# Kernel optimization log

Hardware: AMD Instinct MI355X
Metric: run time of the kernel (lower is better)

## Reference

```python
import jax, jax.numpy as jnp
from jax import lax
import numpy as np

IMG = 640
C = 20  # num_classes
A = 3   # anchors per scale
LB, LO, LC = 0.05, 1.0, 0.5
ANCHORS = jnp.asarray(np.array([[(10, 13), (16, 30), (33, 23)],
                                [(30, 61), (62, 45), (59, 119)],
                                [(116, 90), (156, 198), (373, 326)]], dtype=np.float32) / IMG)


def bce_logits_mean(x, z):
    # BCEWithLogitsLoss (pos_weight=1): mean over all elements, numerically stable
    return jnp.mean(jnp.maximum(x, 0.0) - x * z + jnp.log1p(jnp.exp(-jnp.abs(x))))


def iou_cxcywh(b1, b2, eps=1e-7):
    # b1, b2: [..., 4] in (cx, cy, w, h)
    b1x1 = b1[..., 0] - b1[..., 2] / 2; b1y1 = b1[..., 1] - b1[..., 3] / 2
    b1x2 = b1[..., 0] + b1[..., 2] / 2; b1y2 = b1[..., 1] + b1[..., 3] / 2
    b2x1 = b2[..., 0] - b2[..., 2] / 2; b2y1 = b2[..., 1] - b2[..., 3] / 2
    b2x2 = b2[..., 0] + b2[..., 2] / 2; b2y2 = b2[..., 1] + b2[..., 3] / 2
    iw = jnp.clip(jnp.minimum(b1x2, b2x2) - jnp.maximum(b1x1, b2x1), 0.0)
    ih = jnp.clip(jnp.minimum(b1y2, b2y2) - jnp.maximum(b1y1, b2y1), 0.0)
    inter = iw * ih
    union = (b1x2 - b1x1) * (b1y2 - b1y1) + (b2x2 - b2x1) * (b2y2 - b2y1) - inter + eps
    return inter / union


def build_target(targets, anchors, stride, H, W):
    # targets: [N, T, 6] = (x1, y1, x2, y2, obj, cls); anchors: [A, 2]
    N, T, _ = targets.shape
    x1, y1, x2, y2 = targets[..., 0], targets[..., 1], targets[..., 2], targets[..., 3]
    cls = targets[..., 5]
    valid = (x2 > x1) & (y2 > y1)
    cx = (x1 + x2) * 0.5; cy = (y1 + y2) * 0.5
    bw = x2 - x1; bh = y2 - y1
    gx = jnp.clip(cx / stride, 0.0, W - 1).astype(jnp.int32)  # trunc == floor (nonneg)
    gy = jnp.clip(cy / stride, 0.0, H - 1).astype(jnp.int32)
    dx = cx / stride - gx; dy = cy / stride - gy
    # anchor match: min(r, 1/r) product, argmax over A
    r = jnp.stack([bw[..., None] / anchors[:, 0], bh[..., None] / anchors[:, 1]], axis=-1)  # [N,T,A,2]
    iou_like = jnp.prod(jnp.minimum(r, 1.0 / (r + 1e-6)), axis=-1)  # [N,T,A]
    best = jnp.argmax(iou_like, axis=-1)  # [N,T]
    aw = anchors[best, 0]; ah = anchors[best, 1]
    cls_i = cls.astype(jnp.int32)
    cls_ok = ((cls_i >= 0) & (cls_i < C)).astype(jnp.float32)
    onehot = jax.nn.one_hot(jnp.clip(cls_i, 0, C - 1), C) * cls_ok[..., None]  # [N,T,C]
    vals = jnp.concatenate([
        jnp.stack([dx + 0.5, dy + 0.5, bw / aw, bh / ah, jnp.ones_like(dx)], axis=-1),
        onehot], axis=-1)  # [N,T,5+C]
    tt = jnp.zeros((N, A, 5 + C, H, W), jnp.float32)
    bidx = jnp.arange(N)

    def step(tensor, xs):
        v, gxt, gyt, bt, vt = xs  # per-target slice across the batch, [N,...]
        old = tensor[bidx, bt, :, gyt, gxt]  # [N, 5+C]
        new = jnp.where(vt[:, None], v, old)
        return tensor.at[bidx, bt, :, gyt, gxt].set(new), None

    xs = (jnp.swapaxes(vals, 0, 1), gx.T, gy.T, best.T, valid.T)
    tt, _ = lax.scan(step, tt, xs)
    return tt


def loss_per_scale(pred, targets, scale_idx):
    stride = (8, 16, 32)[scale_idx]
    H = W = IMG // stride
    anchors = ANCHORS[scale_idx]
    N = pred.shape[0]
    tt = build_target(targets, anchors, float(stride), H, W)  # [N,A,5+C,H,W]
    pred = pred.reshape(N, A, 5 + C, H, W)
    ygrid, xgrid = jnp.meshgrid(jnp.arange(H, dtype=jnp.float32),
                                jnp.arange(W, dtype=jnp.float32), indexing='ij')
    grid = jnp.stack([xgrid, ygrid], axis=-1)[None, None]  # [1,1,H,W,2]
    p_txty = jnp.moveaxis(pred[:, :, 0:2], 2, -1)  # [N,A,H,W,2]
    p_twth = jnp.moveaxis(pred[:, :, 2:4], 2, -1)
    p_xy = (2.0 * jax.nn.sigmoid(p_txty) - 0.5 + grid) * stride
    p_wh = (2.0 * jax.nn.sigmoid(p_twth)) ** 2 * anchors.reshape(1, A, 1, 1, 2) * stride
    t_txty = jnp.moveaxis(tt[:, :, 0:2], 2, -1)
    t_twth = jnp.moveaxis(tt[:, :, 2:4], 2, -1)
    t_xy = (t_txty + grid) * stride
    t_wh = t_twth ** 2 * anchors.reshape(1, A, 1, 1, 2)  # NOTE: no *stride, as in source
    pred_box = jnp.concatenate([p_xy, p_wh], axis=-1)
    tgt_box = jnp.concatenate([t_xy, t_wh], axis=-1)
    pos = tt[:, :, 4] == 1.0  # [N,A,H,W]
    npos = jnp.sum(pos)
    ious = iou_cxcywh(pred_box, tgt_box)
    loss_box = jnp.sum((1.0 - ious) * pos) / jnp.maximum(npos, 1).astype(jnp.float32)
    loss_obj = bce_logits_mean(pred[:, :, 4], tt[:, :, 4])
    loss_cls = jnp.where(npos > 0, bce_logits_mean(pred[:, :, 5:], tt[:, :, 5:]), 0.0)
    total = LB * loss_box + LO * loss_obj + LC * loss_cls
    return total, loss_box, loss_obj, loss_cls


def setup_inputs() -> dict:
    key = jax.random.key(0)
    k = jax.random.split(key, 7)
    N, T = 32, 60
    p0 = jax.random.normal(k[0], (N, 75, 80, 80), jnp.float32)
    p1 = jax.random.normal(k[1], (N, 75, 40, 40), jnp.float32)
    p2 = jax.random.normal(k[2], (N, 75, 20, 20), jnp.float32)
    cxy = jax.random.uniform(k[3], (N, T, 2)) * IMG
    wh = jax.random.uniform(k[4], (N, T, 2)) * 120.0 + 8.0
    cls = jax.random.randint(k[5], (N, T), 0, C).astype(jnp.float32)
    x1 = jnp.clip(cxy[..., 0] - wh[..., 0] / 2, 0.0, IMG)
    x2 = jnp.clip(cxy[..., 0] + wh[..., 0] / 2, 0.0, IMG)
    y1 = jnp.clip(cxy[..., 1] - wh[..., 1] / 2, 0.0, IMG)
    y2 = jnp.clip(cxy[..., 1] + wh[..., 1] / 2, 0.0, IMG)
    targets = jnp.stack([x1, y1, x2, y2, jnp.ones_like(x1), cls], axis=-1)
    return {"p0": p0, "p1": p1, "p2": p2, "targets": targets}


def reference(p0, p1, p2, targets):
    total = jnp.float32(0.0)
    lb = jnp.float32(0.0); lo = jnp.float32(0.0); lc = jnp.float32(0.0)
    for i, p in enumerate((p0, p1, p2)):  # 3 structurally distinct scales
        t, b, o, c = loss_per_scale(p, targets, i)
        total = total + t; lb = lb + b; lo = lo + o; lc = lc + c
    return total, lb, lo, lc
```

## Files before the change

kernel.cpp:

```cpp
#include <hip/hip_runtime.h>


#define NB 32
#define NT 60
#define NC 20
#define THREADS 256

#define TGTB 96
#define DM  288
#define DP0 1344
#define DP1 288
#define DENSB (DM + DP0 + DP1)
#define PB0 2240
#define PB12 2100

#define WS_DENSE 384

__constant__ float c_anch[3][3][2] = {
  {{10.f/640.f, 13.f/640.f}, {16.f/640.f, 30.f/640.f}, {33.f/640.f, 23.f/640.f}},
  {{30.f/640.f, 61.f/640.f}, {62.f/640.f, 45.f/640.f}, {59.f/640.f, 119.f/640.f}},
  {{116.f/640.f, 90.f/640.f}, {156.f/640.f, 198.f/640.f}, {373.f/640.f, 326.f/640.f}},
};

__device__ __forceinline__ float sigm(float x) {
  return 1.f / (1.f + __expf(-x));
}
__device__ __forceinline__ float spf(float x) {
  return 1.f + __expf(-fabsf(x));
}
__device__ __forceinline__ float relu4(float4 v) {
  return (fmaxf(v.x, 0.f) + fmaxf(v.y, 0.f)) + (fmaxf(v.z, 0.f) + fmaxf(v.w, 0.f));
}
__device__ __forceinline__ float prod4(float4 v) {
  return (spf(v.x) * spf(v.y)) * (spf(v.z) * spf(v.w));
}

template<int HW, bool MIXED, int PB>
__device__ void sum_dense(const float* __restrict__ bp, int sub,
                          float* __restrict__ outp) {
  const int OBJ4 = HW / 4;
  const int FULLOBJ = OBJ4 >> 8;
  const int BLIM = OBJ4 & 255;
  int tid = threadIdx.x;
  int k0 = (MIXED ? 0 : sub * PB) + tid;
  float4 v[8];
#pragma unroll
  for (int u = 0; u < 8; ++u)
    v[u] = *reinterpret_cast<const float4*>(bp + 4 * (k0 + u * 256));
  const int TAIL = PB - 2048;
  bool hasTail = tid < TAIL;
  float4 vt = make_float4(0.f, 0.f, 0.f, 0.f);
  if (hasTail) vt = *reinterpret_cast<const float4*>(bp + 4 * (k0 + 2048));

  float reluO = 0.f, prodO = 1.f;
  float reluC = 0.f, prodC = 1.f;
#pragma unroll
  for (int u = 0; u < 8; ++u) {
    float r = relu4(v[u]);
    float pr = prod4(v[u]);
    if (MIXED && u < FULLOBJ) {
      reluO += r; prodO *= pr;
    } else if (MIXED && u == FULLOBJ) {
      bool isO = tid < BLIM;
      reluO += isO ? r : 0.f;
      reluC += isO ? 0.f : r;
      prodO *= isO ? pr : 1.f;
      prodC *= isO ? 1.f : pr;
    } else {
      reluC += r; prodC *= pr;
    }
  }
  {
    reluC += relu4(vt);
    prodC *= hasTail ? prod4(vt) : 1.f;
  }
  float accO = MIXED ? (reluO + __logf(prodO)) : 0.f;
  float accC = reluC + __logf(prodC);
#pragma unroll
  for (int o = 32; o > 0; o >>= 1) {
    if (MIXED) accO += __shfl_down(accO, o, 64);
    accC += __shfl_down(accC, o, 64);
  }
  __shared__ float sO[4], sC[4];
  int wid = threadIdx.x >> 6, lane = threadIdx.x & 63;
  if (lane == 0) { sO[wid] = accO; sC[wid] = accC; }
  __syncthreads();
  if (threadIdx.x == 0) {
    outp[0] = MIXED ? (sO[0] + sO[1] + sO[2] + sO[3]) : 0.f;
    outp[1] = sC[0] + sC[1] + sC[2] + sC[3];
  }
}

__device__ void target_block(const float* __restrict__ pred,
                             const float* __restrict__ tg,
                             int scale, int n, float* __restrict__ outp) {
  const int strd = 8 << scale;
  const int W = 80 >> scale;
  const int HW = W * W;
  __shared__ int s_key[64];
  __shared__ int s_val[64];
  int t = threadIdx.x;
  float boxterm = 0.f, objc = 0.f, clsc = 0.f, npos = 0.f;
  float bw = 0.f, bh = 0.f, dx = 0.f, dy = 0.f, clsf = 0.f;
  int gx = 0, gy = 0, best = 0;
  bool valid = false;
  if (t < 64) {
    if (t < NT) {
      const float* g = tg + ((size_t)n * NT + t) * 6;
      float x1 = g[0], y1 = g[1], x2 = g[2], y2 = g[3];
      clsf = g[5];
      valid = (x2 > x1) && (y2 > y1);
      float cx = (x1 + x2) * 0.5f, cy = (y1 + y2) * 0.5f;
      bw = x2 - x1; bh = y2 - y1;
      float fs = (float)strd;
      float gxf = cx / fs, gyf = cy / fs;
      float wm1 = (float)(W - 1);
      gx = (int)fminf(fmaxf(gxf, 0.f), wm1);
      gy = (int)fminf(fmaxf(gyf, 0.f), wm1);
      dx = gxf - (float)gx;
      dy = gyf - (float)gy;
      float bi = -1e30f;
      for (int a = 0; a < 3; a++) {
        float aw = c_anch[scale][a][0], ah = c_anch[scale][a][1];
        float rw = bw / aw, rh = bh / ah;
        float il = fminf(rw, 1.f / (rw + 1e-6f)) * fminf(rh, 1.f / (rh + 1e-6f));
        if (il > bi) { bi = il; best = a; }
      }
      s_key[t] = (best * W + gy) * W + gx;
      s_val[t] = valid ? 1 : 0;
    } else {
      s_key[t] = -1; s_val[t] = 0;
    }
  }
  __syncthreads();
  if (t < NT && valid) {
    bool win = true;
    int key = s_key[t];
    for (int u = t + 1; u < NT; ++u)
      if (s_val[u] && s_key[u] == key) { win = false; break; }
    if (win) {
      float aw = c_anch[scale][best][0], ah = c_anch[scale][best][1];
      const float* base = pred + (size_t)(n * 75 + best * 25) * HW + gy * W + gx;
      float tx = base[0];
      float ty = base[HW];
      float tw = base[2 * HW];
      float th = base[3 * HW];
      float ob = base[4 * HW];
      int clsi = (int)clsf;
      bool clsok = (clsi >= 0) && (clsi < NC);
      int clscl = clsi < 0 ? 0 : (clsi > NC - 1 ? NC - 1 : clsi);
      float cv = base[(5 + clscl) * HW];
      float fs = (float)strd;
      float px = (2.f * sigm(tx) - 0.5f + (float)gx) * fs;
      float py = (2.f * sigm(ty) - 0.5f + (float)gy) * fs;
      float sw = 2.f * sigm(tw); float pw = sw * sw * aw * fs;
      float sh = 2.f * sigm(th); float ph = sh * sh * ah * fs;
      float qx = ((dx + 0.5f) + (float)gx) * fs;
      float qy = ((dy + 0.5f) + (float)gy) * fs;
      float rw = bw / aw; float qw = rw * rw * aw;
      float rh = bh / ah; float qh = rh * rh * ah;
      float b1x1 = px - pw * 0.5f, b1x2 = px + pw * 0.5f;
      float b1y1 = py - ph * 0.5f, b1y2 = py + ph * 0.5f;
      float b2x1 = qx - qw * 0.5f, b2x2 = qx + qw * 0.5f;
      float b2y1 = qy - qh * 0.5f, b2y2 = qy + qh * 0.5f;
      float iw = fmaxf(fminf(b1x2, b2x2) - fmaxf(b1x1, b2x1), 0.f);
      float ih = fmaxf(fminf(b1y2, b2y2) - fmaxf(b1y1, b2y1), 0.f);
      float inter = iw * ih;
      float uni = (b1x2 - b1x1) * (b1y2 - b1y1)
                + (b2x2 - b2x1) * (b2y2 - b2y1) - inter + 1e-7f;
      float iou = inter / uni;
      boxterm = 1.f - iou;
      objc = -ob;
      clsc = clsok ? -cv : 0.f;
      npos = 1.f;
    }
  }
  if (t < 64) {
#pragma unroll
    for (int o = 32; o > 0; o >>= 1) {
      boxterm += __shfl_down(boxterm, o, 64);
      objc    += __shfl_down(objc, o, 64);
      clsc    += __shfl_down(clsc, o, 64);
      npos    += __shfl_down(npos, o, 64);
    }
    if (t == 0) {
      outp[0] = boxterm; outp[1] = objc; outp[2] = clsc; outp[3] = npos;
    }
  }
}

__global__ __launch_bounds__(THREADS)
void yolo_main(const float* __restrict__ p0, const float* __restrict__ p1,
               const float* __restrict__ p2, const float* __restrict__ tg,
               float* __restrict__ ws) {
  int b = blockIdx.x;
  if (b < TGTB) {
    int scale = b / NB, n = b - scale * NB;
    const float* p = scale == 0 ? p0 : (scale == 1 ? p1 : p2);
    target_block(p, tg, scale, n, ws + 4 * (size_t)b);
    return;
  }
  int d = b - TGTB;
  float* outp = ws + WS_DENSE + 2 * (size_t)d;
  if (d < 96) {
    int g = d, n = g / 3, a = g - n * 3;
    sum_dense<6400, true, PB0>(p0 + (size_t)(n * 75 + a * 25 + 4) * 6400, 0, outp);
  } else if (d < 192) {
    int g = d - 96, n = g / 3, a = g - n * 3;
    sum_dense<1600, true, PB12>(p1 + (size_t)(n * 75 + a * 25 + 4) * 1600, 0, outp);
  } else if (d < DM) {
    int g = d - 192, n = g / 3, a = g - n * 3;
    sum_dense<400, true, PB12>(p2 + (size_t)(n * 75 + a * 25 + 4) * 400, 0, outp);
  } else if (d < DM + DP0) {
    int q = d - DM;
    int g = q / 14, sub = 1 + (q - g * 14);
    int n = g / 3, a = g - n * 3;
    sum_dense<6400, false, PB0>(p0 + (size_t)(n * 75 + a * 25 + 4) * 6400, sub, outp);
  } else {
    int q = d - (DM + DP0);
    int g = q / 3, sub = 1 + (q - g * 3);
    int n = g / 3, a = g - n * 3;
    sum_dense<1600, false, PB12>(p1 + (size_t)(n * 75 + a * 25 + 4) * 1600, sub, outp);
  }
}

__device__ __forceinline__ int slot_scale(int d) {
  return d < 96 ? 0 : (d < 192 ? 1 : (d < DM ? 2 : (d < DM + DP0 ? 0 : 1)));
}
__global__ __launch_bounds__(THREADS)
void yolo_final(const float* __restrict__ ws, float* __restrict__ out) {
  int t = threadIdx.x;
  float2 dv[8];
#pragma unroll
  for (int r = 0; r < 7; ++r)
    dv[r] = *reinterpret_cast<const float2*>(ws + WS_DENSE + 2 * (size_t)(t + 256 * r));
  bool has7 = t < DENSB - 1792;
  dv[7] = make_float2(0.f, 0.f);
  if (has7)
    dv[7] = *reinterpret_cast<const float2*>(ws + WS_DENSE + 2 * (size_t)(t + 1792));
  float4 tv = make_float4(0.f, 0.f, 0.f, 0.f);
  if (t < TGTB)
    tv = *reinterpret_cast<const float4*>(ws + 4 * (size_t)t);

  float acc[18];
#pragma unroll
  for (int k = 0; k < 18; k++) acc[k] = 0.f;
#pragma unroll
  for (int r = 0; r < 8; ++r) {
    int s = slot_scale(t + 256 * r);
    acc[2 * s] += dv[r].x;
    acc[2 * s + 1] += dv[r].y;
  }
  if (t < TGTB) {
    int s = t / NB;
    acc[6 + 4 * s + 0] += tv.x;
    acc[6 + 4 * s + 1] += tv.y;
    acc[6 + 4 * s + 2] += tv.z;
    acc[6 + 4 * s + 3] += tv.w;
  }
#pragma unroll
  for (int o = 32; o > 0; o >>= 1)
#pragma unroll
    for (int k = 0; k < 18; k++) acc[k] += __shfl_down(acc[k], o, 64);
  __shared__ float red[4][18];
  int wid = t >> 6, lane = t & 63;
  if (lane == 0)
#pragma unroll
    for (int k = 0; k < 18; k++) red[wid][k] = acc[k];
  __syncthreads();
  if (t == 0) {
    float r[18];
#pragma unroll
    for (int k = 0; k < 18; k++)
      r[k] = red[0][k] + red[1][k] + red[2][k] + red[3][k];
    const float objDen[3] = {614400.f, 153600.f, 38400.f};
    float total = 0.f, lb = 0.f, lo = 0.f, lc = 0.f;
    for (int s = 0; s < 3; s++) {
      float np = r[6 + 4 * s + 3];
      float lbs = r[6 + 4 * s + 0] / fmaxf(np, 1.f);
      float los = (r[2 * s] + r[6 + 4 * s + 1]) / objDen[s];
      float lcs = (np > 0.f)
                    ? (r[2 * s + 1] + r[6 + 4 * s + 2]) / (objDen[s] * (float)NC)
                    : 0.f;
      total += 0.05f * lbs + 1.0f * los + 0.5f * lcs;
      lb += lbs; lo += los; lc += lcs;
    }
    out[0] = total; out[1] = lb; out[2] = lo; out[3] = lc;
  }
}

extern "C" void kernel_launch(void* const* d_in, const int* in_sizes, int n_in,
                              void* d_out, int out_size, void* d_ws, size_t ws_size,
                              hipStream_t stream) {
  const float* p0 = (const float*)d_in[0];
  const float* p1 = (const float*)d_in[1];
  const float* p2 = (const float*)d_in[2];
  const float* tg = (const float*)d_in[3];
  float* ws = (float*)d_ws;
  yolo_main<<<TGTB + DENSB, THREADS, 0, stream>>>(p0, p1, p2, tg, ws);
  yolo_final<<<1, THREADS, 0, stream>>>(ws, (float*)d_out);
}
```

Baseline: 21.46 us.

## Fuse final reduction into main kernel via per-block completion flags

Removes the second kernel launch by adding one extra block that spins on per-producer completion flags in the workspace and then runs the final reduction. Producer blocks publish their partial sums with relaxed agent-scope atomic stores, then set a flag after waiting for their stores to drain. This saves a kernel launch boundary, but it adds a hipMemsetAsync on the flags (another queued operation). It also relies on the finalizer block being scheduled and on relaxed ordering plus vmcnt being enough for visibility.

```diff
diff --git a/kernel.cpp b/kernel.cpp
--- a/kernel.cpp
+++ b/kernel.cpp
@@ -11,10 +11,14 @@
 #define DP0 1344
 #define DP1 288
 #define DENSB (DM + DP0 + DP1)
+#define PRODB (TGTB + DENSB)
 #define PB0 2240
 #define PB12 2100
 
 #define WS_DENSE 384
+#define WS_FLAGS 4224
+
+#define SCOPE_AGENT __HIP_MEMORY_SCOPE_AGENT
 
 __constant__ float c_anch[3][3][2] = {
   {{10.f/640.f, 13.f/640.f}, {16.f/640.f, 30.f/640.f}, {33.f/640.f, 23.f/640.f}},
@@ -33,6 +37,16 @@
 }
 __device__ __forceinline__ float prod4(float4 v) {
   return (spf(v.x) * spf(v.y)) * (spf(v.z) * spf(v.w));
+}
+__device__ __forceinline__ void store2_rlx(float* p, float a, float b) {
+  union { float f[2]; unsigned long long u; } pk;
+  pk.f[0] = a; pk.f[1] = b;
+  __hip_atomic_store((unsigned long long*)p, pk.u, __ATOMIC_RELAXED, SCOPE_AGENT);
+}
+__device__ __forceinline__ float2 load2_rlx(const float* p) {
+  union { unsigned long long u; float f[2]; } pk;
+  pk.u = __hip_atomic_load((const unsigned long long*)p, __ATOMIC_RELAXED, SCOPE_AGENT);
+  return make_float2(pk.f[0], pk.f[1]);
 }
 
 template<int HW, bool MIXED, int PB>
@@ -85,10 +99,9 @@
   int wid = threadIdx.x >> 6, lane = threadIdx.x & 63;
   if (lane == 0) { sO[wid] = accO; sC[wid] = accC; }
   __syncthreads();
-  if (threadIdx.x == 0) {
-    outp[0] = MIXED ? (sO[0] + sO[1] + sO[2] + sO[3]) : 0.f;
-    outp[1] = sC[0] + sC[1] + sC[2] + sC[3];
-  }
+  if (threadIdx.x == 0)
+    store2_rlx(outp, MIXED ? (sO[0] + sO[1] + sO[2] + sO[3]) : 0.f,
+                     sC[0] + sC[1] + sC[2] + sC[3]);
 }
 
 __device__ void target_block(const float* __restrict__ pred,
@@ -184,64 +197,49 @@
       npos    += __shfl_down(npos, o, 64);
     }
     if (t == 0) {
-      outp[0] = boxterm; outp[1] = objc; outp[2] = clsc; outp[3] = npos;
-    }
-  }
-}
-
-__global__ __launch_bounds__(THREADS)
-void yolo_main(const float* __restrict__ p0, const float* __restrict__ p1,
-               const float* __restrict__ p2, const float* __restrict__ tg,
-               float* __restrict__ ws) {
-  int b = blockIdx.x;
-  if (b < TGTB) {
-    int scale = b / NB, n = b - scale * NB;
-    const float* p = scale == 0 ? p0 : (scale == 1 ? p1 : p2);
-    target_block(p, tg, scale, n, ws + 4 * (size_t)b);
-    return;
-  }
-  int d = b - TGTB;
-  float* outp = ws + WS_DENSE + 2 * (size_t)d;
-  if (d < 96) {
-    int g = d, n = g / 3, a = g - n * 3;
-    sum_dense<6400, true, PB0>(p0 + (size_t)(n * 75 + a * 25 + 4) * 6400, 0, outp);
-  } else if (d < 192) {
-    int g = d - 96, n = g / 3, a = g - n * 3;
-    sum_dense<1600, true, PB12>(p1 + (size_t)(n * 75 + a * 25 + 4) * 1600, 0, outp);
-  } else if (d < DM) {
-    int g = d - 192, n = g / 3, a = g - n * 3;
-    sum_dense<400, true, PB12>(p2 + (size_t)(n * 75 + a * 25 + 4) * 400, 0, outp);
-  } else if (d < DM + DP0) {
-    int q = d - DM;
-    int g = q / 14, sub = 1 + (q - g * 14);
-    int n = g / 3, a = g - n * 3;
-    sum_dense<6400, false, PB0>(p0 + (size_t)(n * 75 + a * 25 + 4) * 6400, sub, outp);
-  } else {
-    int q = d - (DM + DP0);
-    int g = q / 3, sub = 1 + (q - g * 3);
-    int n = g / 3, a = g - n * 3;
-    sum_dense<1600, false, PB12>(p1 + (size_t)(n * 75 + a * 25 + 4) * 1600, sub, outp);
+      store2_rlx(outp, boxterm, objc);
+      store2_rlx(outp + 2, clsc, npos);
+    }
   }
 }
 
 __device__ __forceinline__ int slot_scale(int d) {
   return d < 96 ? 0 : (d < 192 ? 1 : (d < DM ? 2 : (d < DM + DP0 ? 0 : 1)));
 }
-__global__ __launch_bounds__(THREADS)
-void yolo_final(const float* __restrict__ ws, float* __restrict__ out) {
+
+__device__ void finalize(const float* __restrict__ ws, float* __restrict__ out,
+                         const unsigned int* __restrict__ flags) {
   int t = threadIdx.x;
+  __shared__ int s_w[4];
+  __shared__ int s_go;
+  while (true) {
+    bool ok = true;
+#pragma unroll
+    for (int r = 0; r < 8; ++r) {
+      int idx = t + 256 * r;
+      if (idx < PRODB)
+        ok &= (__hip_atomic_load(&flags[idx], __ATOMIC_RELAXED, SCOPE_AGENT) != 0u);
+    }
+    unsigned long long ball = __ballot(ok);
+    if ((t & 63) == 0) s_w[t >> 6] = (ball == ~0ull) ? 1 : 0;
+    __syncthreads();
+    if (t == 0) s_go = s_w[0] & s_w[1] & s_w[2] & s_w[3];
+    __syncthreads();
+    if (s_go) break;
+  }
+  __builtin_amdgcn_sched_barrier(0);
   float2 dv[8];
 #pragma unroll
   for (int r = 0; r < 7; ++r)
-    dv[r] = *reinterpret_cast<const float2*>(ws + WS_DENSE + 2 * (size_t)(t + 256 * r));
+    dv[r] = load2_rlx(ws + WS_DENSE + 2 * (size_t)(t + 256 * r));
   bool has7 = t < DENSB - 1792;
   dv[7] = make_float2(0.f, 0.f);
-  if (has7)
-    dv[7] = *reinterpret_cast<const float2*>(ws + WS_DENSE + 2 * (size_t)(t + 1792));
-  float4 tv = make_float4(0.f, 0.f, 0.f, 0.f);
-  if (t < TGTB)
-    tv = *reinterpret_cast<const float4*>(ws + 4 * (size_t)t);
-
+  if (has7) dv[7] = load2_rlx(ws + WS_DENSE + 2 * (size_t)(t + 1792));
+  float2 ta = make_float2(0.f, 0.f), tb = make_float2(0.f, 0.f);
+  if (t < TGTB) {
+    ta = load2_rlx(ws + 4 * (size_t)t);
+    tb = load2_rlx(ws + 4 * (size_t)t + 2);
+  }
   float acc[18];
 #pragma unroll
   for (int k = 0; k < 18; k++) acc[k] = 0.f;
@@ -253,10 +251,10 @@
   }
   if (t < TGTB) {
     int s = t / NB;
-    acc[6 + 4 * s + 0] += tv.x;
-    acc[6 + 4 * s + 1] += tv.y;
-    acc[6 + 4 * s + 2] += tv.z;
-    acc[6 + 4 * s + 3] += tv.w;
+    acc[6 + 4 * s + 0] += ta.x;
+    acc[6 + 4 * s + 1] += ta.y;
+    acc[6 + 4 * s + 2] += tb.x;
+    acc[6 + 4 * s + 3] += tb.y;
   }
 #pragma unroll
   for (int o = 32; o > 0; o >>= 1)
@@ -289,6 +287,50 @@
   }
 }
 
+__global__ __launch_bounds__(THREADS)
+void yolo_main(const float* __restrict__ p0, const float* __restrict__ p1,
+               const float* __restrict__ p2, const float* __restrict__ tg,
+               float* __restrict__ ws, float* __restrict__ out) {
+  int b = blockIdx.x;
+  unsigned int* flags = (unsigned int*)(ws + WS_FLAGS);
+  if (b == PRODB) {
+    finalize(ws, out, flags);
+    return;
+  }
+  if (b < TGTB) {
+    int scale = b / NB, n = b - scale * NB;
+    const float* p = scale == 0 ? p0 : (scale == 1 ? p1 : p2);
+    target_block(p, tg, scale, n, ws + 4 * (size_t)b);
+  } else {
+    int d = b - TGTB;
+    float* outp = ws + WS_DENSE + 2 * (size_t)d;
+    if (d < 96) {
+      int g = d, n = g / 3, a = g - n * 3;
+      sum_dense<6400, true, PB0>(p0 + (size_t)(n * 75 + a * 25 + 4) * 6400, 0, outp);
+    } else if (d < 192) {
+      int g = d - 96, n = g / 3, a = g - n * 3;
+      sum_dense<1600, true, PB12>(p1 + (size_t)(n * 75 + a * 25 + 4) * 1600, 0, outp);
+    } else if (d < DM) {
+      int g = d - 192, n = g / 3, a = g - n * 3;
+      sum_dense<400, true, PB12>(p2 + (size_t)(n * 75 + a * 25 + 4) * 400, 0, outp);
+    } else if (d < DM + DP0) {
+      int q = d - DM;
+      int g = q / 14, sub = 1 + (q - g * 14);
+      int n = g / 3, a = g - n * 3;
+      sum_dense<6400, false, PB0>(p0 + (size_t)(n * 75 + a * 25 + 4) * 6400, sub, outp);
+    } else {
+      int q = d - (DM + DP0);
+      int g = q / 3, sub = 1 + (q - g * 3);
+      int n = g / 3, a = g - n * 3;
+      sum_dense<1600, false, PB12>(p1 + (size_t)(n * 75 + a * 25 + 4) * 1600, sub, outp);
+    }
+  }
+  if (threadIdx.x == 0) {
+    asm volatile("s_waitcnt vmcnt(0)" ::: "memory");
+    __hip_atomic_store(&flags[b], 1u, __ATOMIC_RELAXED, SCOPE_AGENT);
+  }
+}
+
 extern "C" void kernel_launch(void* const* d_in, const int* in_sizes, int n_in,
                               void* d_out, int out_size, void* d_ws, size_t ws_size,
                               hipStream_t stream) {
@@ -297,6 +339,6 @@
   const float* p2 = (const float*)d_in[2];
   const float* tg = (const float*)d_in[3];
   float* ws = (float*)d_ws;
-  yolo_main<<<TGTB + DENSB, THREADS, 0, stream>>>(p0, p1, p2, tg, ws);
-  yolo_final<<<1, THREADS, 0, stream>>>(ws, (float*)d_out);
-}
+  hipMemsetAsync(ws + WS_FLAGS, 0, PRODB * sizeof(unsigned int), stream);
+  yolo_main<<<PRODB + 1, THREADS, 0, stream>>>(p0, p1, p2, tg, ws, (float*)d_out);
+}
```

Measured after the change: 27.71 us. 1.29x slower.
